# Kernel optimization log

Hardware: AMD Instinct MI355X
Metric: run time of the kernel (lower is better)

The kernel has to match this reference:

```python
import jax, jax.numpy as jnp
import numpy as np

B, I, P, H = 256, 1024, 128, 128
L_PROT = 1024
ATOMS_PER_MOL = 128
N_LIG = B * ATOMS_PER_MOL  # 32768 total ligand atoms


def setup_inputs() -> dict:
    key = jax.random.key(0)
    ks = jax.random.split(key, 6)
    param_enc = jax.random.normal(ks[0], (B, I, P), dtype=jnp.float32)
    h_prot = jax.random.normal(ks[1], (B, L_PROT, H), dtype=jnp.float32)
    w1 = jax.random.normal(ks[2], (P, 1), dtype=jnp.float32) / np.sqrt(P)
    b1 = jax.random.normal(ks[3], (1,), dtype=jnp.float32)
    indices_lig = jax.random.randint(ks[4], (B, I), 0, ATOMS_PER_MOL)
    indices_prot = jax.random.randint(ks[5], (B, I), 0, L_PROT)
    protein_idx = jnp.arange(B)            # complex b -> protein row b
    lig_offsets = jnp.arange(B) * ATOMS_PER_MOL  # 'split' cumulative atom offsets
    mask = jnp.ones((B, I), dtype=bool)    # valid (non -510 padded) interactions
    return {
        "param_enc": param_enc, "h_prot": h_prot, "w1": w1, "b1": b1,
        "indices_lig": indices_lig, "indices_prot": indices_prot,
        "protein_idx": protein_idx, "lig_offsets": lig_offsets, "mask": mask,
    }


def reference(param_enc, h_prot, w1, b1, indices_lig, indices_prot,
              protein_idx, lig_offsets, mask):
    # scalar gate per interaction: ReLU(Linear(param_enc))  (dropout = identity, eval mode)
    gate = jax.nn.relu(jnp.einsum("bip,po->bio", param_enc, w1) + b1)  # [B, I, 1]
    # gather protein residue features: h_prot[protein_idx[b], indices_prot[b,i], :]
    gathered = h_prot[protein_idx[:, None], indices_prot]              # [B, I, H]
    contrib = gate * gathered * mask[..., None]                        # [B, I, H]
    # scatter-add into per-ligand-atom accumulator at split + i_l
    glob = (lig_offsets[:, None] + indices_lig).reshape(-1)            # [B*I]
    protein_inter = jnp.zeros((N_LIG, H), dtype=contrib.dtype)
    protein_inter = protein_inter.at[glob].add(contrib.reshape(-1, H))
    return protein_inter
```

## Files before the change

kernel.cpp:

```cpp
#include <hip/hip_runtime.h>

#define B_ 256
#define I_ 1024
#define P_ 128
#define H_ 128
#define LP_ 1024

__global__ __launch_bounds__(256) void gates_k(
    const float* __restrict__ pe,
    const float* __restrict__ w1,
    const float* __restrict__ b1,
    float* __restrict__ gates)
{
    const int tid  = threadIdx.x;
    const int lane = tid & 63;
    const int wv   = tid >> 6;
    const int sub  = lane & 31;
    const int half = lane >> 5;

    const int wave_id   = blockIdx.x * 4 + wv;
    const int item_base = wave_id * 64;

    const float  bias = b1[0];
    const float4 wq   = *(const float4*)(w1 + sub * 4);
    const float* src  = pe + (size_t)item_base * P_;

    #pragma unroll
    for (int u = 0; u < 8; ++u) {
        float4 pv[4];
        #pragma unroll
        for (int j = 0; j < 4; ++j) {
            const int pair = u * 4 + j;
            pv[j] = *(const float4*)(src + (size_t)pair * 256 + lane * 4);
        }
        #pragma unroll
        for (int j = 0; j < 4; ++j) {
            float part = pv[j].x * wq.x + pv[j].y * wq.y
                       + pv[j].z * wq.z + pv[j].w * wq.w;
            part += __shfl_xor(part, 1);
            part += __shfl_xor(part, 2);
            part += __shfl_xor(part, 4);
            part += __shfl_xor(part, 8);
            part += __shfl_xor(part, 16);
            const float gate = fmaxf(part + bias, 0.f);
            if (sub == 0)
                gates[item_base + (u * 4 + j) * 2 + half] = gate;
        }
    }
}

__global__ __launch_bounds__(1024) void scatter_k(
    const float* __restrict__ h_prot,
    const float* __restrict__ gates,
    const int* __restrict__ indices_lig,
    const int* __restrict__ indices_prot,
    const int* __restrict__ protein_idx,
    const int* __restrict__ lig_offsets,
    float* __restrict__ out)
{
    __shared__ float  acc[128 * 128];
    __shared__ float2 live[I_ + 64];
    __shared__ int    nlive;

    const int tid  = threadIdx.x;
    const int b    = blockIdx.x;
    const int lane = tid & 63;
    const int wave = tid >> 6;

    if (tid == 0) nlive = 0;
    float4* acc4 = (float4*)acc;
    for (int k = tid; k < 128 * 128 / 4; k += 1024)
        acc4[k] = make_float4(0.f, 0.f, 0.f, 0.f);
    __syncthreads();

    {
        const float g  = gates[b * I_ + tid];
        const int   il = indices_lig[b * I_ + tid];
        const int   ip = indices_prot[b * I_ + tid];
        const bool pred = g > 0.f;
        const unsigned long long mask = __ballot(pred);
        int base = 0;
        if (lane == 0) base = atomicAdd(&nlive, __popcll(mask));
        base = __shfl(base, 0);
        if (pred) {
            const int pos = base + __popcll(mask & ((1ull << lane) - 1ull));
            live[pos] = make_float2(g, __int_as_float((il << 10) | ip));
        }
    }
    __syncthreads();

    const int n    = nlive;
    const int padN = (n + 63) & ~63;
    for (int k = n + tid; k < padN; k += 1024)
        live[k] = make_float2(0.f, __int_as_float(0));
    __syncthreads();

    const float* hp = h_prot + (size_t)protein_idx[b] * (LP_ * H_);
    const int K = padN >> 4;
    __builtin_assume((K & 3) == 0);
    #pragma unroll 4
    for (int k = 0; k < K; ++k) {
        const float2 m = live[k * 16 + wave];
        const float g  = m.x;
        const int   pk = __float_as_int(m.y);
        const int   il = pk >> 10;
        const int   ip = pk & 1023;
        const float* hr = hp + (size_t)ip * H_;
        const float v0 = hr[lane];
        const float v1 = hr[lane + 64];
        float* ar = acc + il * H_;
        atomicAdd(ar + lane,      g * v0);
        atomicAdd(ar + lane + 64, g * v1);
    }
    __syncthreads();

    const int base = lig_offsets[b];
    float4* out4 = (float4*)(out + (size_t)base * H_);
    for (int k = tid; k < 128 * 128 / 4; k += 1024)
        out4[k] = acc4[k];
}

extern "C" void kernel_launch(void* const* d_in, const int* in_sizes, int n_in,
                              void* d_out, int out_size, void* d_ws, size_t ws_size,
                              hipStream_t stream) {
    const float* param_enc   = (const float*)d_in[0];
    const float* h_prot      = (const float*)d_in[1];
    const float* w1          = (const float*)d_in[2];
    const float* b1          = (const float*)d_in[3];
    const int* indices_lig   = (const int*)d_in[4];
    const int* indices_prot  = (const int*)d_in[5];
    const int* protein_idx   = (const int*)d_in[6];
    const int* lig_offsets   = (const int*)d_in[7];
    float* out   = (float*)d_out;
    float* gates = (float*)d_ws;

    gates_k<<<1024, 256, 0, stream>>>(param_enc, w1, b1, gates);
    scatter_k<<<B_, 1024, 0, stream>>>(h_prot, gates, indices_lig, indices_prot,
                                       protein_idx, lig_offsets, out);
}
```

Measured before the change: 313.0 us.

## Fuse gate computation into scatter kernel and software-pipeline row gathers

Computes the ReLU gates for each batch inside the scatter block and keeps them in shared memory, which removes the separate gates kernel, its launch, and the global round-trip for the gate buffer. The scatter loop is also restructured so the next live row's h_prot values are loaded while the current row is accumulated with LDS atomics. The tradeoff is that the gate GEMV now runs on only 256 blocks of 1024 threads, so far fewer waves are streaming param_enc than the 1024-block launch had. The extra padding of the live list covers the one-ahead prefetch.

```diff
diff --git a/kernel.cpp b/kernel.cpp
--- a/kernel.cpp
+++ b/kernel.cpp
@@ -6,52 +6,11 @@
 #define H_ 128
 #define LP_ 1024
 
-__global__ __launch_bounds__(256) void gates_k(
+__global__ __launch_bounds__(1024) void fused_ile(
     const float* __restrict__ pe,
+    const float* __restrict__ h_prot,
     const float* __restrict__ w1,
     const float* __restrict__ b1,
-    float* __restrict__ gates)
-{
-    const int tid  = threadIdx.x;
-    const int lane = tid & 63;
-    const int wv   = tid >> 6;
-    const int sub  = lane & 31;
-    const int half = lane >> 5;
-
-    const int wave_id   = blockIdx.x * 4 + wv;
-    const int item_base = wave_id * 64;
-
-    const float  bias = b1[0];
-    const float4 wq   = *(const float4*)(w1 + sub * 4);
-    const float* src  = pe + (size_t)item_base * P_;
-
-    #pragma unroll
-    for (int u = 0; u < 8; ++u) {
-        float4 pv[4];
-        #pragma unroll
-        for (int j = 0; j < 4; ++j) {
-            const int pair = u * 4 + j;
-            pv[j] = *(const float4*)(src + (size_t)pair * 256 + lane * 4);
-        }
-        #pragma unroll
-        for (int j = 0; j < 4; ++j) {
-            float part = pv[j].x * wq.x + pv[j].y * wq.y
-                       + pv[j].z * wq.z + pv[j].w * wq.w;
-            part += __shfl_xor(part, 1);
-            part += __shfl_xor(part, 2);
-            part += __shfl_xor(part, 4);
-            part += __shfl_xor(part, 8);
-            part += __shfl_xor(part, 16);
-            const float gate = fmaxf(part + bias, 0.f);
-            if (sub == 0)
-                gates[item_base + (u * 4 + j) * 2 + half] = gate;
-        }
-    }
-}
-
-__global__ __launch_bounds__(1024) void scatter_k(
-    const float* __restrict__ h_prot,
-    const float* __restrict__ gates,
     const int* __restrict__ indices_lig,
     const int* __restrict__ indices_prot,
     const int* __restrict__ protein_idx,
@@ -59,22 +18,56 @@
     float* __restrict__ out)
 {
     __shared__ float  acc[128 * 128];
-    __shared__ float2 live[I_ + 64];
+    __shared__ float  gbuf[I_];
+    __shared__ float2 live[I_ + 128];
     __shared__ int    nlive;
 
     const int tid  = threadIdx.x;
     const int b    = blockIdx.x;
     const int lane = tid & 63;
     const int wave = tid >> 6;
+    const int sub  = lane & 31;
+    const int half = lane >> 5;
 
     if (tid == 0) nlive = 0;
     float4* acc4 = (float4*)acc;
-    for (int k = tid; k < 128 * 128 / 4; k += 1024)
-        acc4[k] = make_float4(0.f, 0.f, 0.f, 0.f);
+    #pragma unroll
+    for (int k = 0; k < 4; ++k)
+        acc4[k * 1024 + tid] = make_float4(0.f, 0.f, 0.f, 0.f);
+
+    {
+        const float  bias = b1[0];
+        const float4 wq   = *(const float4*)(w1 + sub * 4);
+        const int    ibase = wave * 64;
+        const float* src   = pe + (size_t)(b * I_ + ibase) * P_;
+
+        #pragma unroll
+        for (int u = 0; u < 8; ++u) {
+            float4 pv[4];
+            #pragma unroll
+            for (int j = 0; j < 4; ++j) {
+                const int pair = u * 4 + j;
+                pv[j] = *(const float4*)(src + (size_t)pair * 256 + lane * 4);
+            }
+            #pragma unroll
+            for (int j = 0; j < 4; ++j) {
+                float part = pv[j].x * wq.x + pv[j].y * wq.y
+                           + pv[j].z * wq.z + pv[j].w * wq.w;
+                part += __shfl_xor(part, 1);
+                part += __shfl_xor(part, 2);
+                part += __shfl_xor(part, 4);
+                part += __shfl_xor(part, 8);
+                part += __shfl_xor(part, 16);
+                const float gate = fmaxf(part + bias, 0.f);
+                if (sub == 0)
+                    gbuf[ibase + (u * 4 + j) * 2 + half] = gate;
+            }
+        }
+    }
     __syncthreads();
 
     {
-        const float g  = gates[b * I_ + tid];
+        const float g  = gbuf[tid];
         const int   il = indices_lig[b * I_ + tid];
         const int   ip = indices_prot[b * I_ + tid];
         const bool pred = g > 0.f;
@@ -91,33 +84,41 @@
 
     const int n    = nlive;
     const int padN = (n + 63) & ~63;
-    for (int k = n + tid; k < padN; k += 1024)
+    for (int k = n + tid; k < padN + 64; k += 1024)
         live[k] = make_float2(0.f, __int_as_float(0));
     __syncthreads();
 
     const float* hp = h_prot + (size_t)protein_idx[b] * (LP_ * H_);
     const int K = padN >> 4;
-    __builtin_assume((K & 3) == 0);
-    #pragma unroll 4
-    for (int k = 0; k < K; ++k) {
-        const float2 m = live[k * 16 + wave];
-        const float g  = m.x;
-        const int   pk = __float_as_int(m.y);
-        const int   il = pk >> 10;
-        const int   ip = pk & 1023;
-        const float* hr = hp + (size_t)ip * H_;
-        const float v0 = hr[lane];
-        const float v1 = hr[lane + 64];
-        float* ar = acc + il * H_;
-        atomicAdd(ar + lane,      g * v0);
-        atomicAdd(ar + lane + 64, g * v1);
+
+    float2 mcur = live[wave];
+    {
+        const int ip0 = __float_as_int(mcur.y) & 1023;
+        const float* hr = hp + (size_t)ip0 * H_;
+        float v0 = hr[lane];
+        float v1 = hr[lane + 64];
+        #pragma unroll 2
+        for (int k = 0; k < K; ++k) {
+            const float2 mnxt = live[(k + 1) * 16 + wave];
+            const int ipn = __float_as_int(mnxt.y) & 1023;
+            const float* hrn = hp + (size_t)ipn * H_;
+            const float n0 = hrn[lane];
+            const float n1 = hrn[lane + 64];
+            const float g  = mcur.x;
+            const int   il = __float_as_int(mcur.y) >> 10;
+            float* ar = acc + il * H_;
+            atomicAdd(ar + lane,      g * v0);
+            atomicAdd(ar + lane + 64, g * v1);
+            mcur = mnxt; v0 = n0; v1 = n1;
+        }
     }
     __syncthreads();
 
     const int base = lig_offsets[b];
     float4* out4 = (float4*)(out + (size_t)base * H_);
-    for (int k = tid; k < 128 * 128 / 4; k += 1024)
-        out4[k] = acc4[k];
+    #pragma unroll
+    for (int k = 0; k < 4; ++k)
+        out4[k * 1024 + tid] = acc4[k * 1024 + tid];
 }
 
 extern "C" void kernel_launch(void* const* d_in, const int* in_sizes, int n_in,
@@ -131,10 +132,9 @@
     const int* indices_prot  = (const int*)d_in[5];
     const int* protein_idx   = (const int*)d_in[6];
     const int* lig_offsets   = (const int*)d_in[7];
-    float* out   = (float*)d_out;
-    float* gates = (float*)d_ws;
+    float* out = (float*)d_out;
 
-    gates_k<<<1024, 256, 0, stream>>>(param_enc, w1, b1, gates);
-    scatter_k<<<B_, 1024, 0, stream>>>(h_prot, gates, indices_lig, indices_prot,
+    fused_ile<<<B_, 1024, 0, stream>>>(param_enc, h_prot, w1, b1,
+                                       indices_lig, indices_prot,
                                        protein_idx, lig_offsets, out);
 }
```

After: 308.6 us. No clear change (-1.4%).
